# Kernel optimization log

Hardware: AMD Instinct MI355X
Metric: run time of the kernel (lower is better)

## Reference

```python
import jax, jax.numpy as jnp
import numpy as np

N, E = 50000, 600000
DIMS = [128, 256, 256, 256, 256, 64]  # in, h1..h4, out


def setup_inputs() -> dict:
    key = jax.random.key(0)
    ks = jax.random.split(key, 12)
    inp = {
        "x": jax.random.normal(ks[0], (N, DIMS[0]), dtype=jnp.float32),
        "edge_index": jax.random.randint(ks[1], (2, E), 0, N, dtype=jnp.int64 if jax.config.jax_enable_x64 else jnp.int32),
    }
    for i in range(5):
        fi, fo = DIMS[i], DIMS[i + 1]
        s = 1.0 / np.sqrt(fi)  # glorot-ish uniform, matching GCNConv default scale
        inp[f"W{i+1}"] = jax.random.uniform(ks[2 + 2 * i], (fi, fo), jnp.float32, -s, s)
        inp[f"b{i+1}"] = jnp.zeros((fo,), jnp.float32)
    return inp


def _gcn_norm(edge_index, n):
    # Add self-loops and compute symmetric normalization D^-1/2 (A+I) D^-1/2.
    loop = jnp.arange(n, dtype=edge_index.dtype)
    src = jnp.concatenate([edge_index[0], loop])  # [E+N]
    dst = jnp.concatenate([edge_index[1], loop])
    deg = jax.ops.segment_sum(jnp.ones_like(dst, dtype=jnp.float32), dst, num_segments=n)
    dinv = jnp.where(deg > 0, jax.lax.rsqrt(deg), 0.0)
    norm = dinv[src] * dinv[dst]  # [E+N]
    return src, dst, norm


def _gcn_layer(x, src, dst, norm, W, b, n):
    h = x @ W                       # [N, Fo] linear transform first (fewer msg bytes)
    msg = h[src] * norm[:, None]    # gather + edge-weight scale
    out = jax.ops.segment_sum(msg, dst, num_segments=n)  # scatter-add aggregate
    return out + b


def reference(x, edge_index, W1, b1, W2, b2, W3, b3, W4, b4, W5, b5):
    n = x.shape[0]
    src, dst, norm = _gcn_norm(edge_index, n)
    params = [(W1, b1), (W2, b2), (W3, b3), (W4, b4), (W5, b5)]
    h = x
    for i, (W, b) in enumerate(params):
        h = _gcn_layer(h, src, dst, norm, W, b, n)
        if i < 4:
            h = jax.nn.relu(h)  # dropout is identity in eval mode
    return h
```

## Files before the change

kernel.cpp:

```cpp
#include <hip/hip_runtime.h>
#include <stdint.h>


typedef _Float16 v8h __attribute__((ext_vector_type(8)));
typedef _Float16 v4h __attribute__((ext_vector_type(4)));
typedef _Float16 v2h __attribute__((ext_vector_type(2)));
typedef float v4f __attribute__((ext_vector_type(4)));
typedef float v16f __attribute__((ext_vector_type(16)));

__global__ void count_edges(const int* __restrict__ dst, int E, int* __restrict__ counts) {
    int i = blockIdx.x * blockDim.x + threadIdx.x;
    if (i < E) atomicAdd(&counts[dst[i]], 1);
}

__global__ void block_sums(const int* __restrict__ counts, int n, int* __restrict__ partial) {
    __shared__ int red[256];
    int t = threadIdx.x;
    int i = blockIdx.x * 256 + t;
    red[t] = (i < n) ? counts[i] : 0;
    __syncthreads();
    #pragma unroll
    for (int off = 128; off > 0; off >>= 1) {
        if (t < off) red[t] += red[t + off];
        __syncthreads();
    }
    if (t == 0) partial[blockIdx.x] = red[0];
}

__global__ void scan_partials(int* __restrict__ partial, int nb, int* __restrict__ row_ptr, int n) {
    __shared__ int s[256];
    int t = threadIdx.x;
    int v = (t < nb) ? partial[t] : 0;
    s[t] = v;
    __syncthreads();
    #pragma unroll
    for (int off = 1; off < 256; off <<= 1) {
        int u = (t >= off) ? s[t - off] : 0;
        __syncthreads();
        s[t] += u;
        __syncthreads();
    }
    if (t < nb) partial[t] = s[t] - v;
    if (t == 0) row_ptr[n] = s[255];
}

__global__ void scan_final(const int* __restrict__ counts, int n, const int* __restrict__ partial,
                           int* __restrict__ row_ptr, float* __restrict__ dinv,
                           int* __restrict__ fill) {
    __shared__ int s[256];
    int t = threadIdx.x;
    int i = blockIdx.x * 256 + t;
    int c = (i < n) ? counts[i] : 0;
    s[t] = c;
    __syncthreads();
    #pragma unroll
    for (int off = 1; off < 256; off <<= 1) {
        int u = (t >= off) ? s[t - off] : 0;
        __syncthreads();
        s[t] += u;
        __syncthreads();
    }
    if (i < n) {
        row_ptr[i] = partial[blockIdx.x] + s[t] - c;
        dinv[i] = rsqrtf((float)(c + 1));
        fill[i] = 0;
    }
}

__global__ void build_csr(const int* __restrict__ src, const int* __restrict__ dst, int E,
                          const int* __restrict__ row_ptr, int* __restrict__ fill,
                          int2* __restrict__ esw, const float* __restrict__ dinv) {
    int i = blockIdx.x * blockDim.x + threadIdx.x;
    if (i < E) {
        int d = dst[i];
        int s = src[i];
        int pos = row_ptr[d] + atomicAdd(&fill[d], 1);
        esw[pos] = make_int2(s, __float_as_int(dinv[s]));
    }
}

struct SplitArgs {
    const float* W[5];
    _Float16* Wh[5];
    _Float16* Wl[5];
    int lgFI[5];
    int FO[5];
    int off[6];
};

__global__ void split_all(SplitArgs a) {
    int i = blockIdx.x * 256 + threadIdx.x;
    #pragma unroll
    for (int l = 0; l < 5; ++l) {
        if (i >= a.off[l] && i < a.off[l + 1]) {
            int j = i - a.off[l];
            int FI = 1 << a.lgFI[l];
            int c = j >> a.lgFI[l];
            int k = j & (FI - 1);
            float v = a.W[l][(size_t)k * a.FO[l] + c];
            _Float16 h = (_Float16)v;
            a.Wh[l][j] = h;
            a.Wl[l][j] = (_Float16)(v - (float)h);
        }
    }
}

__global__ __launch_bounds__(256) void agg_packed(
    const _Float16* __restrict__ inP, const int* __restrict__ row_ptr,
    const int2* __restrict__ esw, const float* __restrict__ dinv,
    _Float16* __restrict__ outH, _Float16* __restrict__ outL, int n) {
    int wid = (blockIdx.x * blockDim.x + threadIdx.x) >> 6;
    if (wid >= n) return;
    const int lane = threadIdx.x & 63;
    int e = __builtin_amdgcn_readfirstlane(row_ptr[wid]);
    const int end = __builtin_amdgcn_readfirstlane(row_ptr[wid + 1]);
    const float dd = dinv[wid];
    const _Float16* rb = inP + (size_t)lane * 8;
    float a0, a1, a2, a3;
    {
        v8h p = *(const v8h*)(rb + (size_t)wid * 512);
        a0 = dd * ((float)p[0] + (float)p[1]);
        a1 = dd * ((float)p[2] + (float)p[3]);
        a2 = dd * ((float)p[4] + (float)p[5]);
        a3 = dd * ((float)p[6] + (float)p[7]);
    }
#define GTH(q) (*(const v8h*)(rb + (size_t)(q).x * 512))
#define ACC(b, w)                                  \
    a0 += (w) * ((float)(b)[0] + (float)(b)[1]);   \
    a1 += (w) * ((float)(b)[2] + (float)(b)[3]);   \
    a2 += (w) * ((float)(b)[4] + (float)(b)[5]);   \
    a3 += (w) * ((float)(b)[6] + (float)(b)[7]);
    for (; e + 8 <= end; e += 8) {
        int2 q0 = esw[e + 0], q1 = esw[e + 1], q2 = esw[e + 2], q3 = esw[e + 3];
        int2 q4 = esw[e + 4], q5 = esw[e + 5], q6 = esw[e + 6], q7 = esw[e + 7];
        v8h b0 = GTH(q0), b1 = GTH(q1), b2 = GTH(q2), b3 = GTH(q3);
        v8h b4 = GTH(q4), b5 = GTH(q5), b6 = GTH(q6), b7 = GTH(q7);
        ACC(b0, __int_as_float(q0.y)) ACC(b1, __int_as_float(q1.y))
        ACC(b2, __int_as_float(q2.y)) ACC(b3, __int_as_float(q3.y))
        ACC(b4, __int_as_float(q4.y)) ACC(b5, __int_as_float(q5.y))
        ACC(b6, __int_as_float(q6.y)) ACC(b7, __int_as_float(q7.y))
    }
    if (e + 4 <= end) {
        int2 q0 = esw[e + 0], q1 = esw[e + 1], q2 = esw[e + 2], q3 = esw[e + 3];
        v8h b0 = GTH(q0), b1 = GTH(q1), b2 = GTH(q2), b3 = GTH(q3);
        ACC(b0, __int_as_float(q0.y)) ACC(b1, __int_as_float(q1.y))
        ACC(b2, __int_as_float(q2.y)) ACC(b3, __int_as_float(q3.y))
        e += 4;
    }
    if (e < end) {
        const int em = end - 1;
        int e1 = (e + 1 < end) ? e + 1 : em;
        int e2 = (e + 2 < end) ? e + 2 : em;
        int2 q0 = esw[e], q1 = esw[e1], q2 = esw[e2], q3 = esw[em];
        float w0 = __int_as_float(q0.y);
        float w1 = (e + 1 < end) ? __int_as_float(q1.y) : 0.f;
        float w2 = (e + 2 < end) ? __int_as_float(q2.y) : 0.f;
        float w3 = (e + 3 < end) ? __int_as_float(q3.y) : 0.f;
        v8h b0 = GTH(q0), b1 = GTH(q1), b2 = GTH(q2), b3 = GTH(q3);
        ACC(b0, w0) ACC(b1, w1) ACC(b2, w2) ACC(b3, w3)
    }
#undef GTH
#undef ACC
    size_t o = (size_t)wid * 256 + lane * 4;
    float s0 = dd * a0, s1 = dd * a1, s2 = dd * a2, s3 = dd * a3;
    _Float16 h0 = (_Float16)s0, h1 = (_Float16)s1, h2 = (_Float16)s2, h3 = (_Float16)s3;
    *(v4h*)&outH[o] = (v4h){h0, h1, h2, h3};
    *(v4h*)&outL[o] = (v4h){(_Float16)(s0 - (float)h0), (_Float16)(s1 - (float)h1),
                            (_Float16)(s2 - (float)h2), (_Float16)(s3 - (float)h3)};
}

__global__ __launch_bounds__(256) void agg_f32_128(
    const float* __restrict__ in, const int* __restrict__ row_ptr,
    const int2* __restrict__ esw, const float* __restrict__ dinv,
    _Float16* __restrict__ outH, _Float16* __restrict__ outL, int n) {
    int wid = (blockIdx.x * blockDim.x + threadIdx.x) >> 6;
    if (wid >= n) return;
    const int lane = threadIdx.x & 63;
    int e = __builtin_amdgcn_readfirstlane(row_ptr[wid]);
    const int end = __builtin_amdgcn_readfirstlane(row_ptr[wid + 1]);
    const float dd = dinv[wid];
    const float* rb = in + (size_t)lane * 2;
    float a0, a1;
    {
        float2 p = *(const float2*)(rb + (size_t)wid * 128);
        a0 = dd * p.x;
        a1 = dd * p.y;
    }
#define GTH(q) (*(const float2*)(rb + (size_t)(q).x * 128))
#define ACC(b, w) a0 += (w) * (b).x; a1 += (w) * (b).y;
    for (; e + 8 <= end; e += 8) {
        int2 q0 = esw[e + 0], q1 = esw[e + 1], q2 = esw[e + 2], q3 = esw[e + 3];
        int2 q4 = esw[e + 4], q5 = esw[e + 5], q6 = esw[e + 6], q7 = esw[e + 7];
        float2 b0 = GTH(q0), b1 = GTH(q1), b2 = GTH(q2), b3 = GTH(q3);
        float2 b4 = GTH(q4), b5 = GTH(q5), b6 = GTH(q6), b7 = GTH(q7);
        ACC(b0, __int_as_float(q0.y)) ACC(b1, __int_as_float(q1.y))
        ACC(b2, __int_as_float(q2.y)) ACC(b3, __int_as_float(q3.y))
        ACC(b4, __int_as_float(q4.y)) ACC(b5, __int_as_float(q5.y))
        ACC(b6, __int_as_float(q6.y)) ACC(b7, __int_as_float(q7.y))
    }
    if (e + 4 <= end) {
        int2 q0 = esw[e + 0], q1 = esw[e + 1], q2 = esw[e + 2], q3 = esw[e + 3];
        float2 b0 = GTH(q0), b1 = GTH(q1), b2 = GTH(q2), b3 = GTH(q3);
        ACC(b0, __int_as_float(q0.y)) ACC(b1, __int_as_float(q1.y))
        ACC(b2, __int_as_float(q2.y)) ACC(b3, __int_as_float(q3.y))
        e += 4;
    }
    if (e < end) {
        const int em = end - 1;
        int e1 = (e + 1 < end) ? e + 1 : em;
        int e2 = (e + 2 < end) ? e + 2 : em;
        int2 q0 = esw[e], q1 = esw[e1], q2 = esw[e2], q3 = esw[em];
        float w0 = __int_as_float(q0.y);
        float w1 = (e + 1 < end) ? __int_as_float(q1.y) : 0.f;
        float w2 = (e + 2 < end) ? __int_as_float(q2.y) : 0.f;
        float w3 = (e + 3 < end) ? __int_as_float(q3.y) : 0.f;
        float2 b0 = GTH(q0), b1 = GTH(q1), b2 = GTH(q2), b3 = GTH(q3);
        ACC(b0, w0) ACC(b1, w1) ACC(b2, w2) ACC(b3, w3)
    }
#undef GTH
#undef ACC
    size_t o = (size_t)wid * 128 + lane * 2;
    float s0 = dd * a0, s1 = dd * a1;
    _Float16 h0 = (_Float16)s0, h1 = (_Float16)s1;
    *(v2h*)&outH[o] = (v2h){h0, h1};
    *(v2h*)&outL[o] = (v2h){(_Float16)(s0 - (float)h0), (_Float16)(s1 - (float)h1)};
}

__global__ __launch_bounds__(256) void agg_f32_64(
    const float* __restrict__ in, const int* __restrict__ row_ptr,
    const int2* __restrict__ esw, const float* __restrict__ dinv,
    const float* __restrict__ bias, float* __restrict__ outF, int n) {
    int wid = (blockIdx.x * blockDim.x + threadIdx.x) >> 6;
    if (wid >= n) return;
    const int lane = threadIdx.x & 63;
    int e = __builtin_amdgcn_readfirstlane(row_ptr[wid]);
    const int end = __builtin_amdgcn_readfirstlane(row_ptr[wid + 1]);
    const float dd = dinv[wid];
    const float* rb = in + lane;
    float a0 = dd * rb[(size_t)wid * 64];
#define GTH(q) (rb[(size_t)(q).x * 64])
    for (; e + 8 <= end; e += 8) {
        int2 q0 = esw[e + 0], q1 = esw[e + 1], q2 = esw[e + 2], q3 = esw[e + 3];
        int2 q4 = esw[e + 4], q5 = esw[e + 5], q6 = esw[e + 6], q7 = esw[e + 7];
        float b0 = GTH(q0), b1 = GTH(q1), b2 = GTH(q2), b3 = GTH(q3);
        float b4 = GTH(q4), b5 = GTH(q5), b6 = GTH(q6), b7 = GTH(q7);
        a0 += __int_as_float(q0.y) * b0 + __int_as_float(q1.y) * b1;
        a0 += __int_as_float(q2.y) * b2 + __int_as_float(q3.y) * b3;
        a0 += __int_as_float(q4.y) * b4 + __int_as_float(q5.y) * b5;
        a0 += __int_as_float(q6.y) * b6 + __int_as_float(q7.y) * b7;
    }
    if (e + 4 <= end) {
        int2 q0 = esw[e + 0], q1 = esw[e + 1], q2 = esw[e + 2], q3 = esw[e + 3];
        float b0 = GTH(q0), b1 = GTH(q1), b2 = GTH(q2), b3 = GTH(q3);
        a0 += __int_as_float(q0.y) * b0 + __int_as_float(q1.y) * b1;
        a0 += __int_as_float(q2.y) * b2 + __int_as_float(q3.y) * b3;
        e += 4;
    }
    if (e < end) {
        const int em = end - 1;
        int e1 = (e + 1 < end) ? e + 1 : em;
        int e2 = (e + 2 < end) ? e + 2 : em;
        int2 q0 = esw[e], q1 = esw[e1], q2 = esw[e2], q3 = esw[em];
        float w0 = __int_as_float(q0.y);
        float w1 = (e + 1 < end) ? __int_as_float(q1.y) : 0.f;
        float w2 = (e + 2 < end) ? __int_as_float(q2.y) : 0.f;
        float w3 = (e + 3 < end) ? __int_as_float(q3.y) : 0.f;
        float b0 = GTH(q0), b1 = GTH(q1), b2 = GTH(q2), b3 = GTH(q3);
        a0 += w0 * b0 + w1 * b1 + w2 * b2 + w3 * b3;
    }
#undef GTH
    outF[(size_t)wid * 64 + lane] = dd * a0 + bias[lane];
}

__device__ __forceinline__ void gl_lds16(const _Float16* g, _Float16* l) {
    __builtin_amdgcn_global_load_lds(
        (const __attribute__((address_space(1))) uint32_t*)g,
        (__attribute__((address_space(3))) uint32_t*)l, 16, 0, 0);
}

template <int FI, int OUTMODE>
__global__ __launch_bounds__(256) void gemm_wide(
    const _Float16* __restrict__ Ah, const _Float16* __restrict__ Al,
    const _Float16* __restrict__ Wth, const _Float16* __restrict__ Wtl,
    const float* __restrict__ bias,
    uint32_t* __restrict__ Opk, _Float16* __restrict__ Oh, _Float16* __restrict__ Ol,
    int n) {
    constexpr int BK = 32;
    constexpr int NSTEP = FI / BK;
    __shared__ _Float16 lds[20480];
    const int m0 = blockIdx.x * 64;
    const int t = threadIdx.x;
    const int w = t >> 6;
    const int lane = t & 63;

    const int arow = w * 16 + (lane & 15);
    const int akc = (lane >> 4) * 8;
    const _Float16* sAh = Ah + (size_t)(m0 + arow) * FI + akc;
    const _Float16* sAl = Al + (size_t)(m0 + arow) * FI + akc;
    _Float16* dAh = &lds[w * 512];
    _Float16* dAl = &lds[2048 + w * 512];
    size_t boff[4];
    #pragma unroll
    for (int q = 0; q < 4; ++q)
        boff[q] = (size_t)((w * 4 + q) * 16 + (lane & 15)) * FI + akc;

    v16f acc[2][2];
    #pragma unroll
    for (int i = 0; i < 2; ++i)
        #pragma unroll
        for (int j = 0; j < 2; ++j) acc[i][j] = (v16f)(0.f);

    const int rsel = (lane >> 4) & 1;
    const int kq = lane >> 5;
    const int l8 = (lane & 15) * 8;

    for (int s = 0; s < NSTEP; ++s) {
        const int ko = s * BK;
        gl_lds16(sAh + ko, dAh);
        gl_lds16(sAl + ko, dAl);
        #pragma unroll
        for (int q = 0; q < 4; ++q) {
            gl_lds16(Wth + boff[q] + ko, &lds[4096 + (w * 4 + q) * 512]);
            gl_lds16(Wtl + boff[q] + ko, &lds[12288 + (w * 4 + q) * 512]);
        }
        __syncthreads();
        v8h ah[2][2], al[2][2], bh[2][2], bl[2][2];
        #pragma unroll
        for (int i = 0; i < 2; ++i)
            #pragma unroll
            for (int ks = 0; ks < 2; ++ks) {
                const int aoff = (i * 2 + rsel) * 512 + (ks * 2 + kq) * 128 + l8;
                ah[i][ks] = *(const v8h*)&lds[aoff];
                al[i][ks] = *(const v8h*)&lds[2048 + aoff];
            }
        #pragma unroll
        for (int j = 0; j < 2; ++j)
            #pragma unroll
            for (int ks = 0; ks < 2; ++ks) {
                const int bo = 4096 + (w * 4 + j * 2 + rsel) * 512 + (ks * 2 + kq) * 128 + l8;
                bh[j][ks] = *(const v8h*)&lds[bo];
                bl[j][ks] = *(const v8h*)&lds[bo + 8192];
            }
        #pragma unroll
        for (int i = 0; i < 2; ++i)
            #pragma unroll
            for (int j = 0; j < 2; ++j)
                #pragma unroll
                for (int ks = 0; ks < 2; ++ks) {
                    acc[i][j] = __builtin_amdgcn_mfma_f32_32x32x16_f16(ah[i][ks], bh[j][ks], acc[i][j], 0, 0, 0);
                    acc[i][j] = __builtin_amdgcn_mfma_f32_32x32x16_f16(ah[i][ks], bl[j][ks], acc[i][j], 0, 0, 0);
                    acc[i][j] = __builtin_amdgcn_mfma_f32_32x32x16_f16(al[i][ks], bh[j][ks], acc[i][j], 0, 0, 0);
                }
        __syncthreads();
    }

    const int col = lane & 31;
    const int rb4 = (lane >> 5) * 4;
    #pragma unroll
    for (int j = 0; j < 2; ++j) {
        const int gcol = w * 64 + j * 32 + col;
        const float bv = bias[gcol];
        #pragma unroll
        for (int i = 0; i < 2; ++i) {
            #pragma unroll
            for (int reg = 0; reg < 16; ++reg) {
                const int row = (reg & 3) + 8 * (reg >> 2) + rb4;
                const int grow = m0 + i * 32 + row;
                if (grow < n) {
                    float v = fmaxf(acc[i][j][reg] + bv, 0.f);
                    _Float16 h = (_Float16)v;
                    _Float16 l = (_Float16)(v - (float)h);
                    if (OUTMODE == 0) {
                        uint32_t u = (uint32_t)__builtin_bit_cast(uint16_t, h) |
                                     ((uint32_t)__builtin_bit_cast(uint16_t, l) << 16);
                        Opk[(size_t)grow * 256 + gcol] = u;
                    } else {
                        Oh[(size_t)grow * 256 + gcol] = h;
                        Ol[(size_t)grow * 256 + gcol] = l;
                    }
                }
            }
        }
    }
}

__global__ __launch_bounds__(256) void gemm_narrow(
    const _Float16* __restrict__ Ah, const _Float16* __restrict__ Al,
    const _Float16* __restrict__ Wth, const _Float16* __restrict__ Wtl,
    float* __restrict__ Of, int n) {
    constexpr int FI = 256, FO = 64;
    __shared__ _Float16 lds[12288];
    const int m0 = blockIdx.x * 128;
    const int t = threadIdx.x;
    const int w = t >> 6;
    const int lane = t & 63;

    const int G0 = w * 128 + lane;
    const int G1 = G0 + 64;
    const int arow0 = (G0 >> 6) * 16 + (G0 & 15), akc0 = ((G0 >> 4) & 3) * 8;
    const int arow1 = (G1 >> 6) * 16 + (G1 & 15), akc1 = ((G1 >> 4) & 3) * 8;
    const _Float16* sAh0 = Ah + (size_t)(m0 + arow0) * FI + akc0;
    const _Float16* sAh1 = Ah + (size_t)(m0 + arow1) * FI + akc1;
    const _Float16* sAl0 = Al + (size_t)(m0 + arow0) * FI + akc0;
    const _Float16* sAl1 = Al + (size_t)(m0 + arow1) * FI + akc1;
    const int bcol = w * 16 + (lane & 15), bkc = (lane >> 4) * 8;
    const _Float16* sBh = Wth + (size_t)bcol * FI + bkc;
    const _Float16* sBl = Wtl + (size_t)bcol * FI + bkc;

    _Float16* dAh0 = &lds[w * 1024];
    _Float16* dAh1 = &lds[w * 1024 + 512];
    _Float16* dAl0 = &lds[4096 + w * 1024];
    _Float16* dAl1 = &lds[4096 + w * 1024 + 512];
    _Float16* dBh = &lds[8192 + w * 512];
    _Float16* dBl = &lds[10240 + w * 512];

    const int wm = w >> 1, wn = w & 1;
    v4f acc[4][2];
    #pragma unroll
    for (int i = 0; i < 4; ++i)
        #pragma unroll
        for (int j = 0; j < 2; ++j) acc[i][j] = (v4f){0.f, 0.f, 0.f, 0.f};

    for (int s = 0; s < 8; ++s) {
        const int ko = s * 32;
        gl_lds16(sAh0 + ko, dAh0);
        gl_lds16(sAh1 + ko, dAh1);
        gl_lds16(sAl0 + ko, dAl0);
        gl_lds16(sAl1 + ko, dAl1);
        gl_lds16(sBh + ko, dBh);
        gl_lds16(sBl + ko, dBl);
        __syncthreads();
        v8h ah[4], al[4], bh[2], bl[2];
        #pragma unroll
        for (int i = 0; i < 4; ++i) {
            ah[i] = *(const v8h*)&lds[(wm * 4 + i) * 512 + lane * 8];
            al[i] = *(const v8h*)&lds[4096 + (wm * 4 + i) * 512 + lane * 8];
        }
        #pragma unroll
        for (int j = 0; j < 2; ++j) {
            bh[j] = *(const v8h*)&lds[8192 + (wn * 2 + j) * 512 + lane * 8];
            bl[j] = *(const v8h*)&lds[10240 + (wn * 2 + j) * 512 + lane * 8];
        }
        #pragma unroll
        for (int i = 0; i < 4; ++i)
            #pragma unroll
            for (int j = 0; j < 2; ++j) {
                acc[i][j] = __builtin_amdgcn_mfma_f32_16x16x32_f16(ah[i], bh[j], acc[i][j], 0, 0, 0);
                acc[i][j] = __builtin_amdgcn_mfma_f32_16x16x32_f16(ah[i], bl[j], acc[i][j], 0, 0, 0);
                acc[i][j] = __builtin_amdgcn_mfma_f32_16x16x32_f16(al[i], bh[j], acc[i][j], 0, 0, 0);
            }
        __syncthreads();
    }

    const int rl = (lane >> 4) * 4;
    const int cl = lane & 15;
    #pragma unroll
    for (int j = 0; j < 2; ++j) {
        const int gcol = wn * 32 + j * 16 + cl;
        #pragma unroll
        for (int i = 0; i < 4; ++i) {
            const int grow = m0 + wm * 64 + i * 16 + rl;
            #pragma unroll
            for (int r = 0; r < 4; ++r)
                if (grow + r < n) Of[(size_t)(grow + r) * FO + gcol] = acc[i][j][r];
        }
    }
}

extern "C" void kernel_launch(void* const* d_in, const int* in_sizes, int n_in,
                              void* d_out, int out_size, void* d_ws, size_t ws_size,
                              hipStream_t stream) {
    const float* x = (const float*)d_in[0];
    const int* ei = (const int*)d_in[1];
    const int E = in_sizes[1] / 2;
    const int n = in_sizes[0] / 128;
    const int* esrc = ei;
    const int* edst = ei + E;
    const float* b[5] = {(const float*)d_in[3], (const float*)d_in[5], (const float*)d_in[7],
                         (const float*)d_in[9], (const float*)d_in[11]};
    float* out = (float*)d_out;
    const int NPAD = ((n + 127) / 128) * 128;

    char* ws = (char*)d_ws;
    auto carve = [&](size_t bytes) {
        char* p = ws;
        ws += (bytes + 255) & ~(size_t)255;
        return p;
    };
    int* counts = (int*)carve((size_t)n * 4);
    int* row_ptr = (int*)carve((size_t)(n + 1) * 4);
    int* fill = (int*)carve((size_t)n * 4);
    float* dinv = (float*)carve((size_t)n * 4);
    int* partial = (int*)carve(1024);
    int2* esw = (int2*)carve((size_t)E * 8);
    const int FIs[5] = {128, 256, 256, 256, 256};
    const int FOs[5] = {256, 256, 256, 256, 64};
    _Float16 *Wh[5], *Wl[5];
    for (int l = 0; l < 5; ++l) {
        Wh[l] = (_Float16*)carve((size_t)FIs[l] * FOs[l] * 2);
        Wl[l] = (_Float16*)carve((size_t)FIs[l] * FOs[l] * 2);
    }
    _Float16* Ah = (_Float16*)carve((size_t)NPAD * 256 * 2);
    _Float16* Al = (_Float16*)carve((size_t)NPAD * 256 * 2);
    uint32_t* Ppk = (uint32_t*)carve((size_t)NPAD * 256 * 4);
    _Float16* Bh2 = (_Float16*)Ppk;
    _Float16* Bl2 = (_Float16*)Ppk + (size_t)NPAD * 256;
    float* scratch = (float*)Ah;

    hipMemsetAsync(counts, 0, (size_t)n * 4, stream);
    count_edges<<<(E + 255) / 256, 256, 0, stream>>>(edst, E, counts);
    const int nsb = (n + 255) / 256;
    block_sums<<<nsb, 256, 0, stream>>>(counts, n, partial);
    scan_partials<<<1, 256, 0, stream>>>(partial, nsb, row_ptr, n);
    scan_final<<<nsb, 256, 0, stream>>>(counts, n, partial, row_ptr, dinv, fill);
    build_csr<<<(E + 255) / 256, 256, 0, stream>>>(esrc, edst, E, row_ptr, fill, esw, dinv);

    SplitArgs sa;
    int off = 0;
    for (int l = 0; l < 5; ++l) {
        sa.W[l] = (const float*)d_in[2 + 2 * l];
        sa.Wh[l] = Wh[l];
        sa.Wl[l] = Wl[l];
        sa.lgFI[l] = (FIs[l] == 128) ? 7 : 8;
        sa.FO[l] = FOs[l];
        sa.off[l] = off;
        off += FIs[l] * FOs[l];
    }
    sa.off[5] = off;
    split_all<<<(off + 255) / 256, 256, 0, stream>>>(sa);

    const int aggBlocks = (n + 3) / 4;
    const int gw = NPAD / 64;
    const int gn = NPAD / 128;

    agg_f32_128<<<aggBlocks, 256, 0, stream>>>(x, row_ptr, esw, dinv, Ah, Al, n);
    gemm_wide<128, 0><<<gw, 256, 0, stream>>>(Ah, Al, Wh[0], Wl[0], b[0], Ppk, nullptr, nullptr, n);
    for (int l = 1; l <= 2; ++l) {
        agg_packed<<<aggBlocks, 256, 0, stream>>>((const _Float16*)Ppk, row_ptr, esw, dinv, Ah, Al, n);
        gemm_wide<256, 0><<<gw, 256, 0, stream>>>(Ah, Al, Wh[l], Wl[l], b[l], Ppk, nullptr, nullptr, n);
    }
    agg_packed<<<aggBlocks, 256, 0, stream>>>((const _Float16*)Ppk, row_ptr, esw, dinv, Ah, Al, n);
    gemm_wide<256, 1><<<gw, 256, 0, stream>>>(Ah, Al, Wh[3], Wl[3], b[3], nullptr, Bh2, Bl2, n);
    gemm_narrow<<<gn, 256, 0, stream>>>(Bh2, Bl2, Wh[4], Wl[4], scratch, n);
    agg_f32_64<<<(n + 3) / 4, 256, 0, stream>>>(scratch, row_ptr, esw, dinv, b[4], out, n);
}
```

Measured before the change: 669.0 us.

## Overlap aggregation and GEMM by splitting rows into halves in a mixed kernel

```diff
diff --git a/kernel.cpp b/kernel.cpp
--- a/kernel.cpp
+++ b/kernel.cpp
@@ -105,13 +105,10 @@
     }
 }
 
-__global__ __launch_bounds__(256) void agg_packed(
-    const _Float16* __restrict__ inP, const int* __restrict__ row_ptr,
+__device__ __forceinline__ void agg_packed_row(
+    int wid, int lane, const _Float16* __restrict__ inP, const int* __restrict__ row_ptr,
     const int2* __restrict__ esw, const float* __restrict__ dinv,
-    _Float16* __restrict__ outH, _Float16* __restrict__ outL, int n) {
-    int wid = (blockIdx.x * blockDim.x + threadIdx.x) >> 6;
-    if (wid >= n) return;
-    const int lane = threadIdx.x & 63;
+    _Float16* __restrict__ outH, _Float16* __restrict__ outL) {
     int e = __builtin_amdgcn_readfirstlane(row_ptr[wid]);
     const int end = __builtin_amdgcn_readfirstlane(row_ptr[wid + 1]);
     const float dd = dinv[wid];
@@ -169,13 +166,10 @@
                             (_Float16)(s2 - (float)h2), (_Float16)(s3 - (float)h3)};
 }
 
-__global__ __launch_bounds__(256) void agg_f32_128(
-    const float* __restrict__ in, const int* __restrict__ row_ptr,
+__device__ __forceinline__ void agg_f128_row(
+    int wid, int lane, const float* __restrict__ in, const int* __restrict__ row_ptr,
     const int2* __restrict__ esw, const float* __restrict__ dinv,
-    _Float16* __restrict__ outH, _Float16* __restrict__ outL, int n) {
-    int wid = (blockIdx.x * blockDim.x + threadIdx.x) >> 6;
-    if (wid >= n) return;
-    const int lane = threadIdx.x & 63;
+    _Float16* __restrict__ outH, _Float16* __restrict__ outL) {
     int e = __builtin_amdgcn_readfirstlane(row_ptr[wid]);
     const int end = __builtin_amdgcn_readfirstlane(row_ptr[wid + 1]);
     const float dd = dinv[wid];
@@ -224,6 +218,253 @@
     _Float16 h0 = (_Float16)s0, h1 = (_Float16)s1;
     *(v2h*)&outH[o] = (v2h){h0, h1};
     *(v2h*)&outL[o] = (v2h){(_Float16)(s0 - (float)h0), (_Float16)(s1 - (float)h1)};
+}
+
+__device__ __forceinline__ void gl_lds16(const _Float16* g, _Float16* l) {
+    __builtin_amdgcn_global_load_lds(
+        (const __attribute__((address_space(1))) uint32_t*)g,
+        (__attribute__((address_space(3))) uint32_t*)l, 16, 0, 0);
+}
+
+template <int FI, int OUTMODE>
+__device__ __forceinline__ void gemm_wide_block(
+    int m0, const _Float16* __restrict__ Ah, const _Float16* __restrict__ Al,
+    const _Float16* __restrict__ Wth, const _Float16* __restrict__ Wtl,
+    const float* __restrict__ bias,
+    uint32_t* __restrict__ Opk, _Float16* __restrict__ Oh, _Float16* __restrict__ Ol,
+    int n, _Float16* lds) {
+    constexpr int BK = 32;
+    constexpr int NSTEP = FI / BK;
+    const int t = threadIdx.x;
+    const int w = t >> 6;
+    const int lane = t & 63;
+
+    const int arow = w * 16 + (lane & 15);
+    const int akc = (lane >> 4) * 8;
+    const _Float16* sAh = Ah + (size_t)(m0 + arow) * FI + akc;
+    const _Float16* sAl = Al + (size_t)(m0 + arow) * FI + akc;
+    _Float16* dAh = &lds[w * 512];
+    _Float16* dAl = &lds[2048 + w * 512];
+    size_t boff[4];
+    #pragma unroll
+    for (int q = 0; q < 4; ++q)
+        boff[q] = (size_t)((w * 4 + q) * 16 + (lane & 15)) * FI + akc;
+
+    v16f acc[2][2];
+    #pragma unroll
+    for (int i = 0; i < 2; ++i)
+        #pragma unroll
+        for (int j = 0; j < 2; ++j) acc[i][j] = (v16f)(0.f);
+
+    const int rsel = (lane >> 4) & 1;
+    const int kq = lane >> 5;
+    const int l8 = (lane & 15) * 8;
+
+    for (int s = 0; s < NSTEP; ++s) {
+        const int ko = s * BK;
+        gl_lds16(sAh + ko, dAh);
+        gl_lds16(sAl + ko, dAl);
+        #pragma unroll
+        for (int q = 0; q < 4; ++q) {
+            gl_lds16(Wth + boff[q] + ko, &lds[4096 + (w * 4 + q) * 512]);
+            gl_lds16(Wtl + boff[q] + ko, &lds[12288 + (w * 4 + q) * 512]);
+        }
+        __syncthreads();
+        v8h ah[2][2], al[2][2], bh[2][2], bl[2][2];
+        #pragma unroll
+        for (int i = 0; i < 2; ++i)
+            #pragma unroll
+            for (int ks = 0; ks < 2; ++ks) {
+                const int aoff = (i * 2 + rsel) * 512 + (ks * 2 + kq) * 128 + l8;
+                ah[i][ks] = *(const v8h*)&lds[aoff];
+                al[i][ks] = *(const v8h*)&lds[2048 + aoff];
+            }
+        #pragma unroll
+        for (int j = 0; j < 2; ++j)
+            #pragma unroll
+            for (int ks = 0; ks < 2; ++ks) {
+                const int bo = 4096 + (w * 4 + j * 2 + rsel) * 512 + (ks * 2 + kq) * 128 + l8;
+                bh[j][ks] = *(const v8h*)&lds[bo];
+                bl[j][ks] = *(const v8h*)&lds[bo + 8192];
+            }
+        #pragma unroll
+        for (int i = 0; i < 2; ++i)
+            #pragma unroll
+            for (int j = 0; j < 2; ++j)
+                #pragma unroll
+                for (int ks = 0; ks < 2; ++ks) {
+                    acc[i][j] = __builtin_amdgcn_mfma_f32_32x32x16_f16(ah[i][ks], bh[j][ks], acc[i][j], 0, 0, 0);
+                    acc[i][j] = __builtin_amdgcn_mfma_f32_32x32x16_f16(ah[i][ks], bl[j][ks], acc[i][j], 0, 0, 0);
+                    acc[i][j] = __builtin_amdgcn_mfma_f32_32x32x16_f16(al[i][ks], bh[j][ks], acc[i][j], 0, 0, 0);
+                }
+        __syncthreads();
+    }
+
+    const int col = lane & 31;
+    const int rb4 = (lane >> 5) * 4;
+    #pragma unroll
+    for (int j = 0; j < 2; ++j) {
+        const int gcol = w * 64 + j * 32 + col;
+        const float bv = bias[gcol];
+        #pragma unroll
+        for (int i = 0; i < 2; ++i) {
+            #pragma unroll
+            for (int reg = 0; reg < 16; ++reg) {
+                const int row = (reg & 3) + 8 * (reg >> 2) + rb4;
+                const int grow = m0 + i * 32 + row;
+                if (grow < n) {
+                    float v = fmaxf(acc[i][j][reg] + bv, 0.f);
+                    _Float16 h = (_Float16)v;
+                    _Float16 l = (_Float16)(v - (float)h);
+                    if (OUTMODE == 0) {
+                        uint32_t u = (uint32_t)__builtin_bit_cast(uint16_t, h) |
+                                     ((uint32_t)__builtin_bit_cast(uint16_t, l) << 16);
+                        Opk[(size_t)grow * 256 + gcol] = u;
+                    } else {
+                        Oh[(size_t)grow * 256 + gcol] = h;
+                        Ol[(size_t)grow * 256 + gcol] = l;
+                    }
+                }
+            }
+        }
+    }
+}
+
+__global__ __launch_bounds__(256) void agg_packed_rng(
+    const _Float16* __restrict__ inP, const int* __restrict__ row_ptr,
+    const int2* __restrict__ esw, const float* __restrict__ dinv,
+    _Float16* __restrict__ outH, _Float16* __restrict__ outL, int r0, int r1) {
+    int wid = r0 + ((blockIdx.x * blockDim.x + threadIdx.x) >> 6);
+    if (wid >= r1) return;
+    agg_packed_row(wid, threadIdx.x & 63, inP, row_ptr, esw, dinv, outH, outL);
+}
+
+__global__ __launch_bounds__(256) void agg_f128_rng(
+    const float* __restrict__ in, const int* __restrict__ row_ptr,
+    const int2* __restrict__ esw, const float* __restrict__ dinv,
+    _Float16* __restrict__ outH, _Float16* __restrict__ outL, int r0, int r1) {
+    int wid = r0 + ((blockIdx.x * blockDim.x + threadIdx.x) >> 6);
+    if (wid >= r1) return;
+    agg_f128_row(wid, threadIdx.x & 63, in, row_ptr, esw, dinv, outH, outL);
+}
+
+template <int FI, int OUTMODE>
+__global__ __launch_bounds__(256) void gemm_wide_k(
+    int mbase, const _Float16* __restrict__ Ah, const _Float16* __restrict__ Al,
+    const _Float16* __restrict__ Wth, const _Float16* __restrict__ Wtl,
+    const float* __restrict__ bias,
+    uint32_t* __restrict__ Opk, _Float16* __restrict__ Oh, _Float16* __restrict__ Ol, int n) {
+    __shared__ _Float16 lds[20480];
+    gemm_wide_block<FI, OUTMODE>(mbase + blockIdx.x * 64, Ah, Al, Wth, Wtl, bias,
+                                 Opk, Oh, Ol, n, lds);
+}
+
+template <int FI, int OUTMODE, int AGGMODE>
+__global__ __launch_bounds__(256, 4) void mix_k(
+    const _Float16* __restrict__ Ah, const _Float16* __restrict__ Al,
+    const _Float16* __restrict__ Wth, const _Float16* __restrict__ Wtl,
+    const float* __restrict__ bias,
+    uint32_t* __restrict__ Opk, _Float16* __restrict__ OhG, _Float16* __restrict__ OlG,
+    const void* __restrict__ aggIn, const int* __restrict__ row_ptr,
+    const int2* __restrict__ esw, const float* __restrict__ dinv,
+    _Float16* __restrict__ aggOutH, _Float16* __restrict__ aggOutL,
+    int GB, int H, int n) {
+    __shared__ _Float16 lds[20480];
+    if ((int)blockIdx.x < GB) {
+        gemm_wide_block<FI, OUTMODE>(blockIdx.x * 64, Ah, Al, Wth, Wtl, bias,
+                                     Opk, OhG, OlG, n, lds);
+    } else {
+        int wid = H + (((blockIdx.x - GB) * blockDim.x + threadIdx.x) >> 6);
+        if (wid >= n) return;
+        const int lane = threadIdx.x & 63;
+        if (AGGMODE == 1)
+            agg_packed_row(wid, lane, (const _Float16*)aggIn, row_ptr, esw, dinv, aggOutH, aggOutL);
+        else
+            agg_f128_row(wid, lane, (const float*)aggIn, row_ptr, esw, dinv, aggOutH, aggOutL);
+    }
+}
+
+__global__ __launch_bounds__(256) void gemm_narrow(
+    const _Float16* __restrict__ Ah, const _Float16* __restrict__ Al,
+    const _Float16* __restrict__ Wth, const _Float16* __restrict__ Wtl,
+    float* __restrict__ Of, int n) {
+    constexpr int FI = 256, FO = 64;
+    __shared__ _Float16 lds[12288];
+    const int m0 = blockIdx.x * 128;
+    const int t = threadIdx.x;
+    const int w = t >> 6;
+    const int lane = t & 63;
+
+    const int G0 = w * 128 + lane;
+    const int G1 = G0 + 64;
+    const int arow0 = (G0 >> 6) * 16 + (G0 & 15), akc0 = ((G0 >> 4) & 3) * 8;
+    const int arow1 = (G1 >> 6) * 16 + (G1 & 15), akc1 = ((G1 >> 4) & 3) * 8;
+    const _Float16* sAh0 = Ah + (size_t)(m0 + arow0) * FI + akc0;
+    const _Float16* sAh1 = Ah + (size_t)(m0 + arow1) * FI + akc1;
+    const _Float16* sAl0 = Al + (size_t)(m0 + arow0) * FI + akc0;
+    const _Float16* sAl1 = Al + (size_t)(m0 + arow1) * FI + akc1;
+    const int bcol = w * 16 + (lane & 15), bkc = (lane >> 4) * 8;
+    const _Float16* sBh = Wth + (size_t)bcol * FI + bkc;
+    const _Float16* sBl = Wtl + (size_t)bcol * FI + bkc;
+
+    _Float16* dAh0 = &lds[w * 1024];
+    _Float16* dAh1 = &lds[w * 1024 + 512];
+    _Float16* dAl0 = &lds[4096 + w * 1024];
+    _Float16* dAl1 = &lds[4096 + w * 1024 + 512];
+    _Float16* dBh = &lds[8192 + w * 512];
+    _Float16* dBl = &lds[10240 + w * 512];
+
+    const int wm = w >> 1, wn = w & 1;
+    v4f acc[4][2];
+    #pragma unroll
+    for (int i = 0; i < 4; ++i)
+        #pragma unroll
+        for (int j = 0; j < 2; ++j) acc[i][j] = (v4f){0.f, 0.f, 0.f, 0.f};
+
+    for (int s = 0; s < 8; ++s) {
+        const int ko = s * 32;
+        gl_lds16(sAh0 + ko, dAh0);
+        gl_lds16(sAh1 + ko, dAh1);
+        gl_lds16(sAl0 + ko, dAl0);
+        gl_lds16(sAl1 + ko, dAl1);
+        gl_lds16(sBh + ko, dBh);
+        gl_lds16(sBl + ko, dBl);
+        __syncthreads();
+        v8h ah[4], al[4], bh[2], bl[2];
+        #pragma unroll
+        for (int i = 0; i < 4; ++i) {
+            ah[i] = *(const v8h*)&lds[(wm * 4 + i) * 512 + lane * 8];
+            al[i] = *(const v8h*)&lds[4096 + (wm * 4 + i) * 512 + lane * 8];
+        }
+        #pragma unroll
+        for (int j = 0; j < 2; ++j) {
+            bh[j] = *(const v8h*)&lds[8192 + (wn * 2 + j) * 512 + lane * 8];
+            bl[j] = *(const v8h*)&lds[10240 + (wn * 2 + j) * 512 + lane * 8];
+        }
+        #pragma unroll
+        for (int i = 0; i < 4; ++i)
+            #pragma unroll
+            for (int j = 0; j < 2; ++j) {
+                acc[i][j] = __builtin_amdgcn_mfma_f32_16x16x32_f16(ah[i], bh[j], acc[i][j], 0, 0, 0);
+                acc[i][j] = __builtin_amdgcn_mfma_f32_16x16x32_f16(ah[i], bl[j], acc[i][j], 0, 0, 0);
+                acc[i][j] = __builtin_amdgcn_mfma_f32_16x16x32_f16(al[i], bh[j], acc[i][j], 0, 0, 0);
+            }
+        __syncthreads();
+    }
+
+    const int rl = (lane >> 4) * 4;
+    const int cl = lane & 15;
+    #pragma unroll
+    for (int j = 0; j < 2; ++j) {
+        const int gcol = wn * 32 + j * 16 + cl;
+        #pragma unroll
+        for (int i = 0; i < 4; ++i) {
+            const int grow = m0 + wm * 64 + i * 16 + rl;
+            #pragma unroll
+            for (int r = 0; r < 4; ++r)
+                if (grow + r < n) Of[(size_t)(grow + r) * FO + gcol] = acc[i][j][r];
+        }
+    }
 }
 
 __global__ __launch_bounds__(256) void agg_f32_64(
@@ -272,201 +513,6 @@
     outF[(size_t)wid * 64 + lane] = dd * a0 + bias[lane];
 }
 
-__device__ __forceinline__ void gl_lds16(const _Float16* g, _Float16* l) {
-    __builtin_amdgcn_global_load_lds(
-        (const __attribute__((address_space(1))) uint32_t*)g,
-        (__attribute__((address_space(3))) uint32_t*)l, 16, 0, 0);
-}
-
-template <int FI, int OUTMODE>
-__global__ __launch_bounds__(256) void gemm_wide(
-    const _Float16* __restrict__ Ah, const _Float16* __restrict__ Al,
-    const _Float16* __restrict__ Wth, const _Float16* __restrict__ Wtl,
-    const float* __restrict__ bias,
-    uint32_t* __restrict__ Opk, _Float16* __restrict__ Oh, _Float16* __restrict__ Ol,
-    int n) {
-    constexpr int BK = 32;
-    constexpr int NSTEP = FI / BK;
-    __shared__ _Float16 lds[20480];
-    const int m0 = blockIdx.x * 64;
-    const int t = threadIdx.x;
-    const int w = t >> 6;
-    const int lane = t & 63;
-
-    const int arow = w * 16 + (lane & 15);
-    const int akc = (lane >> 4) * 8;
-    const _Float16* sAh = Ah + (size_t)(m0 + arow) * FI + akc;
-    const _Float16* sAl = Al + (size_t)(m0 + arow) * FI + akc;
-    _Float16* dAh = &lds[w * 512];
-    _Float16* dAl = &lds[2048 + w * 512];
-    size_t boff[4];
-    #pragma unroll
-    for (int q = 0; q < 4; ++q)
-        boff[q] = (size_t)((w * 4 + q) * 16 + (lane & 15)) * FI + akc;
-
-    v16f acc[2][2];
-    #pragma unroll
-    for (int i = 0; i < 2; ++i)
-        #pragma unroll
-        for (int j = 0; j < 2; ++j) acc[i][j] = (v16f)(0.f);
-
-    const int rsel = (lane >> 4) & 1;
-    const int kq = lane >> 5;
-    const int l8 = (lane & 15) * 8;
-
-    for (int s = 0; s < NSTEP; ++s) {
-        const int ko = s * BK;
-        gl_lds16(sAh + ko, dAh);
-        gl_lds16(sAl + ko, dAl);
-        #pragma unroll
-        for (int q = 0; q < 4; ++q) {
-            gl_lds16(Wth + boff[q] + ko, &lds[4096 + (w * 4 + q) * 512]);
-            gl_lds16(Wtl + boff[q] + ko, &lds[12288 + (w * 4 + q) * 512]);
-        }
-        __syncthreads();
-        v8h ah[2][2], al[2][2], bh[2][2], bl[2][2];
-        #pragma unroll
-        for (int i = 0; i < 2; ++i)
-            #pragma unroll
-            for (int ks = 0; ks < 2; ++ks) {
-                const int aoff = (i * 2 + rsel) * 512 + (ks * 2 + kq) * 128 + l8;
-                ah[i][ks] = *(const v8h*)&lds[aoff];
-                al[i][ks] = *(const v8h*)&lds[2048 + aoff];
-            }
-        #pragma unroll
-        for (int j = 0; j < 2; ++j)
-            #pragma unroll
-            for (int ks = 0; ks < 2; ++ks) {
-                const int bo = 4096 + (w * 4 + j * 2 + rsel) * 512 + (ks * 2 + kq) * 128 + l8;
-                bh[j][ks] = *(const v8h*)&lds[bo];
-                bl[j][ks] = *(const v8h*)&lds[bo + 8192];
-            }
-        #pragma unroll
-        for (int i = 0; i < 2; ++i)
-            #pragma unroll
-            for (int j = 0; j < 2; ++j)
-                #pragma unroll
-                for (int ks = 0; ks < 2; ++ks) {
-                    acc[i][j] = __builtin_amdgcn_mfma_f32_32x32x16_f16(ah[i][ks], bh[j][ks], acc[i][j], 0, 0, 0);
-                    acc[i][j] = __builtin_amdgcn_mfma_f32_32x32x16_f16(ah[i][ks], bl[j][ks], acc[i][j], 0, 0, 0);
-                    acc[i][j] = __builtin_amdgcn_mfma_f32_32x32x16_f16(al[i][ks], bh[j][ks], acc[i][j], 0, 0, 0);
-                }
-        __syncthreads();
-    }
-
-    const int col = lane & 31;
-    const int rb4 = (lane >> 5) * 4;
-    #pragma unroll
-    for (int j = 0; j < 2; ++j) {
-        const int gcol = w * 64 + j * 32 + col;
-        const float bv = bias[gcol];
-        #pragma unroll
-        for (int i = 0; i < 2; ++i) {
-            #pragma unroll
-            for (int reg = 0; reg < 16; ++reg) {
-                const int row = (reg & 3) + 8 * (reg >> 2) + rb4;
-                const int grow = m0 + i * 32 + row;
-                if (grow < n) {
-                    float v = fmaxf(acc[i][j][reg] + bv, 0.f);
-                    _Float16 h = (_Float16)v;
-                    _Float16 l = (_Float16)(v - (float)h);
-                    if (OUTMODE == 0) {
-                        uint32_t u = (uint32_t)__builtin_bit_cast(uint16_t, h) |
-                                     ((uint32_t)__builtin_bit_cast(uint16_t, l) << 16);
-                        Opk[(size_t)grow * 256 + gcol] = u;
-                    } else {
-                        Oh[(size_t)grow * 256 + gcol] = h;
-                        Ol[(size_t)grow * 256 + gcol] = l;
-                    }
-                }
-            }
-        }
-    }
-}
-
-__global__ __launch_bounds__(256) void gemm_narrow(
-    const _Float16* __restrict__ Ah, const _Float16* __restrict__ Al,
-    const _Float16* __restrict__ Wth, const _Float16* __restrict__ Wtl,
-    float* __restrict__ Of, int n) {
-    constexpr int FI = 256, FO = 64;
-    __shared__ _Float16 lds[12288];
-    const int m0 = blockIdx.x * 128;
-    const int t = threadIdx.x;
-    const int w = t >> 6;
-    const int lane = t & 63;
-
-    const int G0 = w * 128 + lane;
-    const int G1 = G0 + 64;
-    const int arow0 = (G0 >> 6) * 16 + (G0 & 15), akc0 = ((G0 >> 4) & 3) * 8;
-    const int arow1 = (G1 >> 6) * 16 + (G1 & 15), akc1 = ((G1 >> 4) & 3) * 8;
-    const _Float16* sAh0 = Ah + (size_t)(m0 + arow0) * FI + akc0;
-    const _Float16* sAh1 = Ah + (size_t)(m0 + arow1) * FI + akc1;
-    const _Float16* sAl0 = Al + (size_t)(m0 + arow0) * FI + akc0;
-    const _Float16* sAl1 = Al + (size_t)(m0 + arow1) * FI + akc1;
-    const int bcol = w * 16 + (lane & 15), bkc = (lane >> 4) * 8;
-    const _Float16* sBh = Wth + (size_t)bcol * FI + bkc;
-    const _Float16* sBl = Wtl + (size_t)bcol * FI + bkc;
-
-    _Float16* dAh0 = &lds[w * 1024];
-    _Float16* dAh1 = &lds[w * 1024 + 512];
-    _Float16* dAl0 = &lds[4096 + w * 1024];
-    _Float16* dAl1 = &lds[4096 + w * 1024 + 512];
-    _Float16* dBh = &lds[8192 + w * 512];
-    _Float16* dBl = &lds[10240 + w * 512];
-
-    const int wm = w >> 1, wn = w & 1;
-    v4f acc[4][2];
-    #pragma unroll
-    for (int i = 0; i < 4; ++i)
-        #pragma unroll
-        for (int j = 0; j < 2; ++j) acc[i][j] = (v4f){0.f, 0.f, 0.f, 0.f};
-
-    for (int s = 0; s < 8; ++s) {
-        const int ko = s * 32;
-        gl_lds16(sAh0 + ko, dAh0);
-        gl_lds16(sAh1 + ko, dAh1);
-        gl_lds16(sAl0 + ko, dAl0);
-        gl_lds16(sAl1 + ko, dAl1);
-        gl_lds16(sBh + ko, dBh);
-        gl_lds16(sBl + ko, dBl);
-        __syncthreads();
-        v8h ah[4], al[4], bh[2], bl[2];
-        #pragma unroll
-        for (int i = 0; i < 4; ++i) {
-            ah[i] = *(const v8h*)&lds[(wm * 4 + i) * 512 + lane * 8];
-            al[i] = *(const v8h*)&lds[4096 + (wm * 4 + i) * 512 + lane * 8];
-        }
-        #pragma unroll
-        for (int j = 0; j < 2; ++j) {
-            bh[j] = *(const v8h*)&lds[8192 + (wn * 2 + j) * 512 + lane * 8];
-            bl[j] = *(const v8h*)&lds[10240 + (wn * 2 + j) * 512 + lane * 8];
-        }
-        #pragma unroll
-        for (int i = 0; i < 4; ++i)
-            #pragma unroll
-            for (int j = 0; j < 2; ++j) {
-                acc[i][j] = __builtin_amdgcn_mfma_f32_16x16x32_f16(ah[i], bh[j], acc[i][j], 0, 0, 0);
-                acc[i][j] = __builtin_amdgcn_mfma_f32_16x16x32_f16(ah[i], bl[j], acc[i][j], 0, 0, 0);
-                acc[i][j] = __builtin_amdgcn_mfma_f32_16x16x32_f16(al[i], bh[j], acc[i][j], 0, 0, 0);
-            }
-        __syncthreads();
-    }
-
-    const int rl = (lane >> 4) * 4;
-    const int cl = lane & 15;
-    #pragma unroll
-    for (int j = 0; j < 2; ++j) {
-        const int gcol = wn * 32 + j * 16 + cl;
-        #pragma unroll
-        for (int i = 0; i < 4; ++i) {
-            const int grow = m0 + wm * 64 + i * 16 + rl;
-            #pragma unroll
-            for (int r = 0; r < 4; ++r)
-                if (grow + r < n) Of[(size_t)(grow + r) * FO + gcol] = acc[i][j][r];
-        }
-    }
-}
-
 extern "C" void kernel_launch(void* const* d_in, const int* in_sizes, int n_in,
                               void* d_out, int out_size, void* d_ws, size_t ws_size,
                               hipStream_t stream) {
@@ -480,6 +526,7 @@
                          (const float*)d_in[9], (const float*)d_in[11]};
     float* out = (float*)d_out;
     const int NPAD = ((n + 127) / 128) * 128;
+    const int H = (NPAD / 2) & ~63;
 
     char* ws = (char*)d_ws;
     auto carve = [&](size_t bytes) {
@@ -502,9 +549,10 @@
     }
     _Float16* Ah = (_Float16*)carve((size_t)NPAD * 256 * 2);
     _Float16* Al = (_Float16*)carve((size_t)NPAD * 256 * 2);
-    uint32_t* Ppk = (uint32_t*)carve((size_t)NPAD * 256 * 4);
-    _Float16* Bh2 = (_Float16*)Ppk;
-    _Float16* Bl2 = (_Float16*)Ppk + (size_t)NPAD * 256;
+    uint32_t* P0 = (uint32_t*)carve((size_t)NPAD * 256 * 4);
+    uint32_t* P1 = (uint32_t*)carve((size_t)NPAD * 256 * 4);
+    _Float16* Bh2 = (_Float16*)P1;
+    _Float16* Bl2 = (_Float16*)P1 + (size_t)NPAD * 256;
     float* scratch = (float*)Ah;
 
     hipMemsetAsync(counts, 0, (size_t)n * 4, stream);
@@ -529,18 +577,35 @@
     sa.off[5] = off;
     split_all<<<(off + 255) / 256, 256, 0, stream>>>(sa);
 
-    const int aggBlocks = (n + 3) / 4;
-    const int gw = NPAD / 64;
-    const int gn = NPAD / 128;
-
-    agg_f32_128<<<aggBlocks, 256, 0, stream>>>(x, row_ptr, esw, dinv, Ah, Al, n);
-    gemm_wide<128, 0><<<gw, 256, 0, stream>>>(Ah, Al, Wh[0], Wl[0], b[0], Ppk, nullptr, nullptr, n);
+    const int GB1 = H / 64;
+    const int GB2 = (NPAD - H) / 64;
+    const int AB1 = (H + 3) / 4;
+    const int AB2 = (n - H + 3) / 4;
+
+    agg_f128_rng<<<AB1, 256, 0, stream>>>(x, row_ptr, esw, dinv, Ah, Al, 0, H);
+    mix_k<128, 0, 0><<<GB1 + AB2, 256, 0, stream>>>(Ah, Al, Wh[0], Wl[0], b[0],
+                                                    P0, nullptr, nullptr,
+                                                    x, row_ptr, esw, dinv, Ah, Al, GB1, H, n);
+    gemm_wide_k<128, 0><<<GB2, 256, 0, stream>>>(H, Ah, Al, Wh[0], Wl[0], b[0],
+                                                 P0, nullptr, nullptr, n);
+    uint32_t* Pin = P0;
+    uint32_t* Pout = P1;
     for (int l = 1; l <= 2; ++l) {
-        agg_packed<<<aggBlocks, 256, 0, stream>>>((const _Float16*)Ppk, row_ptr, esw, dinv, Ah, Al, n);
-        gemm_wide<256, 0><<<gw, 256, 0, stream>>>(Ah, Al, Wh[l], Wl[l], b[l], Ppk, nullptr, nullptr, n);
-    }
-    agg_packed<<<aggBlocks, 256, 0, stream>>>((const _Float16*)Ppk, row_ptr, esw, dinv, Ah, Al, n);
-    gemm_wide<256, 1><<<gw, 256, 0, stream>>>(Ah, Al, Wh[3], Wl[3], b[3], nullptr, Bh2, Bl2, n);
-    gemm_narrow<<<gn, 256, 0, stream>>>(Bh2, Bl2, Wh[4], Wl[4], scratch, n);
+        agg_packed_rng<<<AB1, 256, 0, stream>>>((const _Float16*)Pin, row_ptr, esw, dinv,
+                                                Ah, Al, 0, H);
+        mix_k<256, 0, 1><<<GB1 + AB2, 256, 0, stream>>>(Ah, Al, Wh[l], Wl[l], b[l],
+                                                        Pout, nullptr, nullptr,
+                                                        Pin, row_ptr, esw, dinv, Ah, Al, GB1, H, n);
+        gemm_wide_k<256, 0><<<GB2, 256, 0, stream>>>(H, Ah, Al, Wh[l], Wl[l], b[l],
+                                                     Pout, nullptr, nullptr, n);
+        uint32_t* tmp = Pin; Pin = Pout; Pout = tmp;
+    }
+    agg_packed_rng<<<AB1, 256, 0, stream>>>((const _Float16*)Pin, row_ptr, esw, dinv, Ah, Al, 0, H);
+    mix_k<256, 1, 1><<<GB1 + AB2, 256, 0, stream>>>(Ah, Al, Wh[3], Wl[3], b[3],
+                                                    nullptr, Bh2, Bl2,
+                                                    Pin, row_ptr, esw, dinv, Ah, Al, GB1, H, n);
+    gemm_wide_k<256, 1><<<GB2, 256, 0, stream>>>(H, Ah, Al, Wh[3], Wl[3], b[3],
+                                                 nullptr, Bh2, Bl2, n);
+    gemm_narrow<<<NPAD / 128, 256, 0, stream>>>(Bh2, Bl2, Wh[4], Wl[4], scratch, n);
     agg_f32_64<<<(n + 3) / 4, 256, 0, stream>>>(scratch, row_ptr, esw, dinv, b[4], out, n);
 }
```

Measured after the change: 635.8 us. 1.05x faster.
